# Optimization experiments

Hardware: AMD Instinct MI355X
Metric: run time of the kernel (lower is better)

The kernel has to match this reference:

```python
import jax, jax.numpy as jnp
import numpy as np

B, P, K = 32, 1024, 20  # clouds, points per cloud, kNN neighbors
EPS = 1e-5


def knn_idx(x, k):
    # x: [B,P,d] -> indices of k nearest neighbors (squared L2, includes self), [B,P,k]
    d2 = jnp.sum(x * x, axis=-1)
    dist = d2[:, :, None] + d2[:, None, :] - 2.0 * jnp.einsum('bpd,bqd->bpq', x, x)
    _, idx = jax.lax.top_k(-dist, k)
    return idx


def edge_conv(x, idx, msg_fn):
    # gather neighbor features, build [x_i, x_j - x_i] edge features, max-aggregate
    xj = jax.vmap(lambda xb, ib: xb[ib])(x, idx)            # [B,P,K,d]
    xi = jnp.broadcast_to(x[:, :, None, :], xj.shape)       # [B,P,K,d]
    e = jnp.concatenate([xi, xj - xi], axis=-1)             # [B,P,K,2d]
    return jnp.max(msg_fn(e), axis=2)                       # [B,P,out]


def setup_inputs() -> dict:
    key = jax.random.key(0)
    ks = jax.random.split(key, 5)
    s = 0.05
    return {
        'pos': jax.random.normal(ks[0], (B * P, 3), jnp.float32),
        'W1a': jax.random.normal(ks[1], (6, 64), jnp.float32) * s,
        'b1a': jnp.zeros((64,), jnp.float32),
        'g1': jnp.ones((64,), jnp.float32),
        'be1': jnp.zeros((64,), jnp.float32),
        'W1b': jax.random.normal(ks[2], (64, 64), jnp.float32) * s,
        'b1b': jnp.zeros((64,), jnp.float32),
        'W2': jax.random.normal(ks[3], (128, 128), jnp.float32) * s,
        'b2': jnp.zeros((128,), jnp.float32),
        'Wl': jax.random.normal(ks[4], (192, 128), jnp.float32) * s,
        'bl': jnp.zeros((128,), jnp.float32),
        'batch': jnp.repeat(jnp.arange(B, dtype=jnp.int32), P),
    }


def reference(pos, W1a, b1a, g1, be1, W1b, b1b, W2, b2, Wl, bl, batch):
    # batch is uniform-sized and sorted -> fixed reshape to [B,P,.]
    x0 = pos.reshape(B, P, 3)

    def mlp1(e):  # Linear(6,64) -> BatchNorm -> ReLU -> Linear(64,64)
        h = e @ W1a + b1a
        mu = jnp.mean(h, axis=(0, 1, 2))
        var = jnp.var(h, axis=(0, 1, 2))
        h = (h - mu) * jax.lax.rsqrt(var + EPS) * g1 + be1
        h = jax.nn.relu(h)
        return h @ W1b + b1b

    x1 = edge_conv(x0, knn_idx(x0, K), mlp1)                         # [B,P,64]
    x2 = edge_conv(x1, knn_idx(x1, K), lambda e: e @ W2 + b2)        # [B,P,128]
    h = jnp.concatenate([x1, x2], axis=-1) @ Wl + bl                 # [B,P,128]
    return jnp.max(h, axis=1)                                        # global_max_pool -> [B,128]
```

## Files before the change

kernel.cpp:

```cpp
#include <hip/hip_runtime.h>
#include <cfloat>
#include <cstdint>

#define NB 32
#define NP 1024
#define NK 20
#define NPTS 32768

typedef __attribute__((ext_vector_type(8))) short bf16x8;
typedef __attribute__((ext_vector_type(4))) float f32x4;

__device__ __forceinline__ unsigned bf16rne(float v) {
  const unsigned u = __float_as_uint(v);
  return (u + 0x7fffu + ((u >> 16) & 1u)) >> 16;
}

__global__ __launch_bounds__(256) void kd2(const float* __restrict__ x, int dim,
                                           float* __restrict__ d2) {
  int p = blockIdx.x * 256 + threadIdx.x;
  if (p >= NPTS) return;
  if (dim == 64) {
    const float4* xr = (const float4*)(x + (size_t)p * 64);
    float s = 0.f;
#pragma unroll
    for (int dq = 0; dq < 16; dq++) {
      float4 v = xr[dq];
      s = fmaf(v.x, v.x, s);
      s = fmaf(v.y, v.y, s);
      s = fmaf(v.z, v.z, s);
      s = fmaf(v.w, v.w, s);
    }
    d2[p] = s;
  } else {
    float s = 0.f;
#pragma unroll
    for (int d = 0; d < 3; d++) {
      float v = x[p * 3 + d];
      s = fmaf(v, v, s);
    }
    d2[p] = s;
  }
}

__global__ __launch_bounds__(256) void kxprep(const float* __restrict__ x,
                                              unsigned short* __restrict__ Xh,
                                              unsigned short* __restrict__ Xl) {
  const int t = blockIdx.x * 256 + threadIdx.x;
  const int p = t >> 3, g = t & 7;
  const float4* xr = (const float4*)(x + (size_t)p * 64 + g * 8);
  const float4 v0 = xr[0];
  const float4 v1 = xr[1];
  const float vv[8] = {v0.x, v0.y, v0.z, v0.w, v1.x, v1.y, v1.z, v1.w};
  unsigned short h[8], l[8];
#pragma unroll
  for (int j = 0; j < 8; j++) {
    const float z = vv[j];
    const unsigned u = __float_as_uint(z);
    const unsigned hb = (u + 0x7fffu + ((u >> 16) & 1u)) & 0xffff0000u;
    h[j] = (unsigned short)(hb >> 16);
    l[j] = (unsigned short)bf16rne(z - __uint_as_float(hb));
  }
  const int off = (((p >> 4) * 2 + (g >> 2)) * 64 + ((g & 3) << 4) + (p & 15)) * 8;
  *(uint4*)&Xh[off] = *(const uint4*)&h[0];
  *(uint4*)&Xl[off] = *(const uint4*)&l[0];
}

__global__ __launch_bounds__(256) void kdistm(const unsigned short* __restrict__ Xh,
                                              const unsigned short* __restrict__ Xl,
                                              const float* __restrict__ d2,
                                              int c0, int nc, float* __restrict__ D) {
  const int lane = threadIdx.x & 63;
  const int w = threadIdx.x >> 6;
  const int cloud = blockIdx.x % nc;
  const int t = blockIdx.x / nc;
  const int tr0 = (t >> 3) * 128, tc0 = (t & 7) * 128;
  const int cb = (c0 + cloud) * 1024;
  const int rw = tr0 + w * 32;

  bf16x8 Ah[2][2], Al[2][2];
#pragma unroll
  for (int mt = 0; mt < 2; mt++)
#pragma unroll
    for (int ks = 0; ks < 2; ks++) {
      const int tg = (cb + rw + mt * 16) >> 4;
      const size_t base = ((size_t)(tg * 2 + ks) * 64 + lane) * 8;
      Ah[mt][ks] = *(const bf16x8*)&Xh[base];
      Al[mt][ks] = *(const bf16x8*)&Xl[base];
    }
  float d2r[2][4];
#pragma unroll
  for (int mt = 0; mt < 2; mt++)
#pragma unroll
    for (int r = 0; r < 4; r++)
      d2r[mt][r] = d2[cb + rw + mt * 16 + (lane >> 4) * 4 + r];

  for (int nt = 0; nt < 8; nt++) {
    const int cg = cb + tc0 + nt * 16;
    bf16x8 Bh2[2], Bl2[2];
#pragma unroll
    for (int ks = 0; ks < 2; ks++) {
      const int tg = cg >> 4;
      const size_t base = ((size_t)(tg * 2 + ks) * 64 + lane) * 8;
      Bh2[ks] = *(const bf16x8*)&Xh[base];
      Bl2[ks] = *(const bf16x8*)&Xl[base];
    }
    const float d2c = d2[cg + (lane & 15)];
#pragma unroll
    for (int mt = 0; mt < 2; mt++) {
      f32x4 C = {0.f, 0.f, 0.f, 0.f};
      C = __builtin_amdgcn_mfma_f32_16x16x32_bf16(Ah[mt][0], Bh2[0], C, 0, 0, 0);
      C = __builtin_amdgcn_mfma_f32_16x16x32_bf16(Ah[mt][0], Bl2[0], C, 0, 0, 0);
      C = __builtin_amdgcn_mfma_f32_16x16x32_bf16(Al[mt][0], Bh2[0], C, 0, 0, 0);
      C = __builtin_amdgcn_mfma_f32_16x16x32_bf16(Ah[mt][1], Bh2[1], C, 0, 0, 0);
      C = __builtin_amdgcn_mfma_f32_16x16x32_bf16(Ah[mt][1], Bl2[1], C, 0, 0, 0);
      C = __builtin_amdgcn_mfma_f32_16x16x32_bf16(Al[mt][1], Bh2[1], C, 0, 0, 0);
#pragma unroll
      for (int r = 0; r < 4; r++) {
        const int row = cloud * 1024 + rw + mt * 16 + (lane >> 4) * 4 + r;
        const int col = tc0 + nt * 16 + (lane & 15);
        D[(size_t)row * 1024 + col] = fmaf(-2.f, C[r], d2r[mt][r] + d2c);
      }
    }
  }
}

__device__ __forceinline__ void select20(const float* dv, unsigned long long* w,
                                         int lane, int pg, int gbase,
                                         int* __restrict__ idxo) {
  unsigned k32[16];
#pragma unroll
  for (int ii = 0; ii < 16; ii++) {
    unsigned u = __float_as_uint(dv[ii]);
    u ^= (((int)u >> 31) | 0x80000000u);
    k32[ii] = u;
  }
  unsigned lmn = k32[0];
#pragma unroll
  for (int ii = 1; ii < 16; ii++) lmn = k32[ii] < lmn ? k32[ii] : lmn;
  unsigned mn = lmn, mxm = lmn;
#pragma unroll
  for (int s = 1; s < 64; s <<= 1) {
    const unsigned a = __shfl_xor(mn, s, 64);
    const unsigned b = __shfl_xor(mxm, s, 64);
    mn = a < mn ? a : mn;
    mxm = b > mxm ? b : mxm;
  }
  unsigned lo = mn;
  unsigned long long hi = (unsigned long long)mxm + 1;
  unsigned m32 = 0;
  bool found = false;
  for (int it = 0; it < 34; ++it) {
    if (hi - lo <= 1) break;
    const unsigned m = (unsigned)(lo + ((hi - (unsigned long long)lo) >> 1));
    int cnt = 0;
#pragma unroll
    for (int ii = 0; ii < 16; ii++) cnt += __popcll(__ballot(k32[ii] < m));
    if (cnt < 20)
      lo = m;
    else if (cnt > 63)
      hi = m;
    else {
      m32 = m;
      found = true;
      break;
    }
  }

  if (found) {
    unsigned mask = 0;
    unsigned long long key64[16];
#pragma unroll
    for (int i = 0; i < 4; i++)
#pragma unroll
      for (int j = 0; j < 4; j++) {
        const int ii = i * 4 + j;
        key64[ii] = ((unsigned long long)k32[ii] << 10) |
                    (unsigned)(i * 256 + (lane << 2) + j);
        mask |= (k32[ii] < m32) ? (1u << ii) : 0u;
      }
    const int lc = __popc(mask);
    int x = lc;
#pragma unroll
    for (int s = 1; s < 64; s <<= 1) {
      const int y = __shfl_up(x, s, 64);
      if (lane >= s) x += y;
    }
    int off = x - lc;
    w[lane] = ~0ULL;
    __builtin_amdgcn_wave_barrier();
#pragma unroll
    for (int ii = 0; ii < 16; ii++) {
      if (mask & (1u << ii)) {
        w[off] = key64[ii];
        off++;
      }
    }
    __builtin_amdgcn_wave_barrier();
    const unsigned long long K = w[lane];
    unsigned long long lo64 = ((unsigned long long)lo) << 10;
    unsigned long long hi64 = ((unsigned long long)m32) << 10;
    unsigned long long cut = hi64;
    for (int it = 0; it < 48 && (hi64 - lo64) > 1; ++it) {
      const unsigned long long m = lo64 + ((hi64 - lo64) >> 1);
      const int cnt = __popcll(__ballot(K < m));
      if (cnt == 20) {
        cut = m;
        break;
      }
      if (cnt < 20)
        lo64 = m;
      else
        hi64 = m;
      cut = hi64;
    }
    const unsigned long long sel = __ballot(K < cut);
    if (K < cut) {
      const int slot = __builtin_amdgcn_mbcnt_hi(
          (unsigned)(sel >> 32), __builtin_amdgcn_mbcnt_lo((unsigned)sel, 0));
      idxo[(size_t)pg * NK + slot] = gbase + (int)(K & 1023u);
    }
  } else {
    unsigned long long key64[16];
#pragma unroll
    for (int i = 0; i < 4; i++)
#pragma unroll
      for (int j = 0; j < 4; j++) {
        const int ii = i * 4 + j;
        key64[ii] = ((unsigned long long)k32[ii] << 10) |
                    (unsigned)(i * 256 + (lane << 2) + j);
      }
    unsigned long long lo64 = ((unsigned long long)lo) << 10;
    unsigned long long hi64 = hi << 10;
    unsigned long long cut = hi64;
    for (int it = 0; it < 48 && (hi64 - lo64) > 1; ++it) {
      const unsigned long long m = lo64 + ((hi64 - lo64) >> 1);
      int cnt = 0;
#pragma unroll
      for (int ii = 0; ii < 16; ii++) cnt += __popcll(__ballot(key64[ii] < m));
      if (cnt == 20) {
        cut = m;
        break;
      }
      if (cnt < 20)
        lo64 = m;
      else
        hi64 = m;
      cut = hi64;
    }
    int base = 0;
#pragma unroll
    for (int ii = 0; ii < 16; ii++) {
      const unsigned long long b = __ballot(key64[ii] < cut);
      if (key64[ii] < cut) {
        const int slot = base + __builtin_amdgcn_mbcnt_hi(
                                    (unsigned)(b >> 32),
                                    __builtin_amdgcn_mbcnt_lo((unsigned)b, 0));
        idxo[(size_t)pg * NK + slot] = gbase + (int)(key64[ii] & 1023u);
      }
      base += __popcll(b);
    }
  }
}

__global__ __launch_bounds__(256) void kfsel1(const float* __restrict__ pos,
                                              const float* __restrict__ d2,
                                              int* __restrict__ idxo) {
  __shared__ float px[1024], py[1024], pz[1024], pd2[1024];
  __shared__ unsigned long long lw[4][64];
  const int tid = threadIdx.x;
  const int lane = tid & 63;
  const int w = tid >> 6;
  const int cloud = blockIdx.x >> 6;
  const int mb = blockIdx.x & 63;
  const int cb = cloud << 10;

  {
    const float4* ppos = (const float4*)(pos + (size_t)cb * 3 + tid * 12);
    const float4 a = ppos[0], b = ppos[1], c = ppos[2];
    *(float4*)&px[tid * 4] = make_float4(a.x, a.w, b.z, c.y);
    *(float4*)&py[tid * 4] = make_float4(a.y, b.x, b.w, c.z);
    *(float4*)&pz[tid * 4] = make_float4(a.z, b.y, c.x, c.w);
    *(float4*)&pd2[tid * 4] = *(const float4*)(d2 + cb + tid * 4);
  }
  __syncthreads();

  for (int pp = 0; pp < 4; pp++) {
    const int pl = mb * 16 + w * 4 + pp;
    const float xi0 = px[pl], xi1 = py[pl], xi2 = pz[pl];
    const float dp = pd2[pl];
    float dv[16];
#pragma unroll
    for (int i = 0; i < 4; i++) {
      const float4 X = *(const float4*)&px[i * 256 + lane * 4];
      const float4 Y = *(const float4*)&py[i * 256 + lane * 4];
      const float4 Z = *(const float4*)&pz[i * 256 + lane * 4];
      const float4 Q = *(const float4*)&pd2[i * 256 + lane * 4];
      const float xs[4] = {X.x, X.y, X.z, X.w};
      const float ys[4] = {Y.x, Y.y, Y.z, Y.w};
      const float zs[4] = {Z.x, Z.y, Z.z, Z.w};
      const float qs[4] = {Q.x, Q.y, Q.z, Q.w};
#pragma unroll
      for (int j = 0; j < 4; j++) {
        float acc = 0.f;
        acc = fmaf(xi0, xs[j], acc);
        acc = fmaf(xi1, ys[j], acc);
        acc = fmaf(xi2, zs[j], acc);
        dv[i * 4 + j] = fmaf(-2.f, acc, dp + qs[j]);
      }
    }
    select20(dv, lw[w], lane, cb + pl, cb, idxo);
  }
}

__global__ __launch_bounds__(256) void kselect2(const float* __restrict__ D,
                                                int c0, int* __restrict__ idxo) {
  __shared__ unsigned long long lw[4][64];
  const int lane = threadIdx.x & 63;
  const int sub = threadIdx.x >> 6;
  const int pchunk = blockIdx.x * 4 + sub;
  const int pg = c0 * 1024 + pchunk;
  const int gbase = (pg >> 10) << 10;

  float dv[16];
  const float4* dr = (const float4*)(D + (size_t)pchunk * 1024 + lane * 4);
#pragma unroll
  for (int i = 0; i < 4; i++) {
    const float4 d4 = dr[i * 64];
    dv[i * 4 + 0] = d4.x;
    dv[i * 4 + 1] = d4.y;
    dv[i * 4 + 2] = d4.z;
    dv[i * 4 + 3] = d4.w;
  }
  select20(dv, lw[sub], lane, pg, gbase, idxo);
}

__global__ __launch_bounds__(256) void kstats(const float* __restrict__ pos,
                                              const int* __restrict__ idx,
                                              double* __restrict__ Spart) {
  __shared__ float red[4][42];
  const int tid = threadIdx.x;
  const int w = tid >> 6;
  int p = blockIdx.x * 256 + tid;
  float xi0 = pos[p * 3], xi1 = pos[p * 3 + 1], xi2 = pos[p * 3 + 2];
  float s1[6];
  float s2[36];
#pragma unroll
  for (int a = 0; a < 6; a++) s1[a] = 0.f;
#pragma unroll
  for (int a = 0; a < 36; a++) s2[a] = 0.f;
  for (int k = 0; k < NK; k++) {
    int j = idx[p * NK + k];
    float e[6];
    e[0] = xi0;
    e[1] = xi1;
    e[2] = xi2;
    e[3] = pos[j * 3] - xi0;
    e[4] = pos[j * 3 + 1] - xi1;
    e[5] = pos[j * 3 + 2] - xi2;
#pragma unroll
    for (int a = 0; a < 6; a++) {
      s1[a] += e[a];
#pragma unroll
      for (int b = 0; b < 6; b++) s2[a * 6 + b] = fmaf(e[a], e[b], s2[a * 6 + b]);
    }
  }
#pragma unroll
  for (int a = 0; a < 6; a++) {
#pragma unroll
    for (int m = 1; m < 64; m <<= 1) s1[a] += __shfl_xor(s1[a], m, 64);
  }
#pragma unroll
  for (int a = 0; a < 36; a++) {
#pragma unroll
    for (int m = 1; m < 64; m <<= 1) s2[a] += __shfl_xor(s2[a], m, 64);
  }
  if ((tid & 63) == 0) {
#pragma unroll
    for (int a = 0; a < 6; a++) red[w][a] = s1[a];
#pragma unroll
    for (int a = 0; a < 36; a++) red[w][6 + a] = s2[a];
  }
  __syncthreads();
  if (tid < 42) {
    double t = (double)red[0][tid] + (double)red[1][tid] + (double)red[2][tid] +
               (double)red[3][tid];
    Spart[(size_t)blockIdx.x * 42 + tid] = t;
  }
}

__global__ void kbn(const double* __restrict__ Spart, const float* __restrict__ W1a,
                    const float* __restrict__ b1a, const float* __restrict__ g1,
                    const float* __restrict__ be1, const float* __restrict__ W1b,
                    float* __restrict__ ss, unsigned short* __restrict__ Bh,
                    unsigned short* __restrict__ Bl) {
  __shared__ double S[42];
  const int c = threadIdx.x;
  if (c < 42) {
    double t = 0.0;
    for (int b = 0; b < 128; b++) t += Spart[(size_t)b * 42 + c];
    S[c] = t;
  }
  for (int t = c; t < 4096; t += 256) {
    const int j = t & 7, L = (t >> 3) & 63, f = t >> 9;
    const int nt = f >> 1, ks = f & 1;
    const int k = ks * 32 + (L >> 4) * 8 + j;
    const int n = nt * 16 + (L & 15);
    const float wv = W1b[k * 64 + n];
    const unsigned u = __float_as_uint(wv);
    const unsigned hb = (u + 0x7fffu + ((u >> 16) & 1u)) & 0xffff0000u;
    Bh[t] = (unsigned short)(hb >> 16);
    Bl[t] = (unsigned short)bf16rne(wv - __uint_as_float(hb));
  }
  __syncthreads();
  if (c < 64) {
    double w[6];
#pragma unroll
    for (int d = 0; d < 6; d++) w[d] = (double)W1a[d * 64 + c];
    double b = (double)b1a[c];
    const double invN = 1.0 / (double)((size_t)NPTS * NK);
    double m1 = 0.0;
#pragma unroll
    for (int d = 0; d < 6; d++) m1 += w[d] * S[d];
    m1 *= invN;
    double q = 0.0;
#pragma unroll
    for (int a = 0; a < 6; a++)
#pragma unroll
      for (int d = 0; d < 6; d++) q += w[a] * w[d] * S[6 + a * 6 + d];
    q *= invN;
    double mu = m1 + b;
    double eh2 = q + 2.0 * b * m1 + b * b;
    double var = eh2 - mu * mu;
    if (var < 0.0) var = 0.0;
    double inv = 1.0 / sqrt(var + 1e-5);
    double sc = (double)g1[c] * inv;
    ss[c] = (float)sc;
    ss[64 + c] = (float)((double)be1[c] - mu * sc);
  }
}

#define EC1P 8
__global__ __launch_bounds__(256) void kec1(const float* __restrict__ pos,
                                            const int* __restrict__ idx,
                                            const float* __restrict__ ss,
                                            const float* __restrict__ W1a,
                                            const float* __restrict__ b1a,
                                            const unsigned short* __restrict__ Bh,
                                            const unsigned short* __restrict__ Bl,
                                            const float* __restrict__ b1b,
                                            float* __restrict__ x1) {
  __shared__ __align__(16) unsigned short Ah[4][3072];
  __shared__ __align__(16) unsigned short Al[4][3072];
  __shared__ float nbr[4][160];
  const int tid = threadIdx.x;
  const int lane = tid & 63;
  const int w = tid >> 6;
  const int p0 = blockIdx.x * EC1P + w * 2;

  unsigned short* ah = Ah[w];
  unsigned short* al = Al[w];
  float* nb = nbr[w];

  if (lane < 40) {
    const int j = idx[(size_t)p0 * NK + lane];
    nb[lane * 4 + 0] = pos[j * 3 + 0];
    nb[lane * 4 + 1] = pos[j * 3 + 1];
    nb[lane * 4 + 2] = pos[j * 3 + 2];
  }

  float wdf[3], wbt[3];
#pragma unroll
  for (int d = 0; d < 3; d++) {
    const float top = W1a[d * 64 + lane];
    const float bot = W1a[(3 + d) * 64 + lane];
    wdf[d] = top - bot;
    wbt[d] = bot;
  }
  const float b1 = b1a[lane];
  const float sc = ss[lane];
  const float sh = ss[64 + lane];
  const int lanepart = ((lane >> 5) * 512) + (((lane & 31) >> 3) * 128) + (lane & 7);
  __builtin_amdgcn_wave_barrier();

#pragma unroll
  for (int pp = 0; pp < 2; pp++) {
    const int p = p0 + pp;
    const float xi0 = pos[p * 3], xi1 = pos[p * 3 + 1], xi2 = pos[p * 3 + 2];
    const float pu = fmaf(xi2, wdf[2], fmaf(xi1, wdf[1], fmaf(xi0, wdf[0], b1)));
    for (int k = 0; k < NK; k++) {
      const int row = pp * NK + k;
      const float4 nbv = *(const float4*)&nb[row * 4];
      const float pv = fmaf(nbv.z, wbt[2], fmaf(nbv.y, wbt[1], nbv.x * wbt[0]));
      const float z = fmaxf(fmaf(pu + pv, sc, sh), 0.f);
      const unsigned u = __float_as_uint(z);
      const unsigned hb = (u + 0x7fffu + ((u >> 16) & 1u)) & 0xffff0000u;
      const int off = (row >> 4) * 1024 + (row & 15) * 8 + lanepart;
      ah[off] = (unsigned short)(hb >> 16);
      al[off] = (unsigned short)bf16rne(z - __uint_as_float(hb));
    }
  }
  __builtin_amdgcn_wave_barrier();

  bf16x8 bh[4][2], bl[4][2];
#pragma unroll
  for (int nt = 0; nt < 4; nt++)
#pragma unroll
    for (int ks = 0; ks < 2; ks++) {
      const int base = ((nt * 2 + ks) * 64 + lane) * 8;
      bh[nt][ks] = *(const bf16x8*)&Bh[base];
      bl[nt][ks] = *(const bf16x8*)&Bl[base];
    }

  float pA[4], pB[4];
#pragma unroll
  for (int nt = 0; nt < 4; nt++) {
    pA[nt] = -FLT_MAX;
    pB[nt] = -FLT_MAX;
  }
  const int q4 = (lane >> 4) * 4;

#pragma unroll
  for (int mt = 0; mt < 3; mt++) {
    const bf16x8 a_h0 = *(const bf16x8*)&ah[mt * 1024 + lane * 8];
    const bf16x8 a_l0 = *(const bf16x8*)&al[mt * 1024 + lane * 8];
    const bf16x8 a_h1 = *(const bf16x8*)&ah[mt * 1024 + 512 + lane * 8];
    const bf16x8 a_l1 = *(const bf16x8*)&al[mt * 1024 + 512 + lane * 8];
#pragma unroll
    for (int nt = 0; nt < 4; nt++) {
      f32x4 C = {0.f, 0.f, 0.f, 0.f};
      C = __builtin_amdgcn_mfma_f32_16x16x32_bf16(a_h0, bh[nt][0], C, 0, 0, 0);
      C = __builtin_amdgcn_mfma_f32_16x16x32_bf16(a_h0, bl[nt][0], C, 0, 0, 0);
      C = __builtin_amdgcn_mfma_f32_16x16x32_bf16(a_l0, bh[nt][0], C, 0, 0, 0);
      C = __builtin_amdgcn_mfma_f32_16x16x32_bf16(a_h1, bh[nt][1], C, 0, 0, 0);
      C = __builtin_amdgcn_mfma_f32_16x16x32_bf16(a_h1, bl[nt][1], C, 0, 0, 0);
      C = __builtin_amdgcn_mfma_f32_16x16x32_bf16(a_l1, bh[nt][1], C, 0, 0, 0);
#pragma unroll
      for (int r = 0; r < 4; r++) {
        const int row = mt * 16 + q4 + r;
        const float vv = C[r];
        if (row < NK) pA[nt] = fmaxf(pA[nt], vv);
        if (row >= NK && row < 2 * NK) pB[nt] = fmaxf(pB[nt], vv);
      }
    }
  }
#pragma unroll
  for (int s = 16; s < 64; s <<= 1) {
#pragma unroll
    for (int nt = 0; nt < 4; nt++) {
      pA[nt] = fmaxf(pA[nt], __shfl_xor(pA[nt], s, 64));
      pB[nt] = fmaxf(pB[nt], __shfl_xor(pB[nt], s, 64));
    }
  }
  if (lane < 16) {
#pragma unroll
    for (int nt = 0; nt < 4; nt++) {
      const float bb = b1b[nt * 16 + lane];
      x1[(size_t)p0 * 64 + nt * 16 + lane] = pA[nt] + bb;
      x1[(size_t)(p0 + 1) * 64 + nt * 16 + lane] = pB[nt] + bb;
    }
  }
}

__global__ __launch_bounds__(256) void kv(const float* __restrict__ x1,
                                          const float* __restrict__ W2,
                                          float* __restrict__ v) {
  const int c = threadIdx.x & 127;
  const int sub = threadIdx.x >> 7;
  float wv[64];
#pragma unroll
  for (int d = 0; d < 64; d++) wv[d] = W2[(64 + d) * 128 + c];
  const int pbase = blockIdx.x * 64 + sub * 32;
  for (int i = 0; i < 32; i++) {
    const int p = pbase + i;
    const float4* xr = (const float4*)(x1 + (size_t)p * 64);
    float a0 = 0.f, a1 = 0.f;
#pragma unroll
    for (int dq = 0; dq < 16; dq++) {
      float4 xv = xr[dq];
      a0 = fmaf(xv.x, wv[dq * 4 + 0], a0);
      a1 = fmaf(xv.y, wv[dq * 4 + 1], a1);
      a0 = fmaf(xv.z, wv[dq * 4 + 2], a0);
      a1 = fmaf(xv.w, wv[dq * 4 + 3], a1);
    }
    v[(size_t)p * 128 + c] = a0 + a1;
  }
}

__global__ __launch_bounds__(256) void kprep(const float* __restrict__ W2,
                                             const float* __restrict__ Wl,
                                             const float* __restrict__ b2,
                                             const float* __restrict__ bl,
                                             float* __restrict__ Bc,
                                             float* __restrict__ cb) {
  const int t = blockIdx.x * 256 + threadIdx.x;
  const int d = t >> 7, c = t & 127;
  float s = Wl[d * 128 + c];
  for (int e = 0; e < 128; e++)
    s = fmaf(W2[d * 128 + e] - W2[(64 + d) * 128 + e], Wl[(64 + e) * 128 + c], s);
  Bc[d * 128 + c] = s;
  Bc[(64 + 2 * d) * 128 + c] = Wl[(64 + 2 * d) * 128 + c];
  Bc[(64 + 2 * d + 1) * 128 + c] = Wl[(64 + 2 * d + 1) * 128 + c];
  if (d == 0) {
    float sb = bl[c];
    for (int e = 0; e < 128; e++) sb = fmaf(b2[e], Wl[(64 + e) * 128 + c], sb);
    cb[c] = sb;
  }
}

#define ATS 72
#define BSS 132
__global__ __launch_bounds__(256) void kgemm(const float* __restrict__ x1,
                                             const float* __restrict__ v,
                                             const int* __restrict__ idx,
                                             const float* __restrict__ Bc,
                                             float* __restrict__ partial) {
  __shared__ float AT[192 * ATS];
  __shared__ float BS[16 * BSS];
  int* idxs = (int*)BS;
  const int tid = threadIdx.x;
  const int cloud = blockIdx.x & 31;
  const int mb = blockIdx.x >> 5;
  const int pbase = cloud * 1024 + mb * 64;

#pragma unroll
  for (int r = 0; r < 5; r++) {
    int id = r * 256 + tid;
    idxs[id] = idx[(size_t)pbase * NK + id];
  }
#pragma unroll
  for (int r = 0; r < 16; r++) {
    int id = r * 256 + tid;
    int m = id >> 6, k = id & 63;
    AT[k * ATS + m] = x1[(size_t)(pbase + m) * 64 + k];
  }
  __syncthreads();
#pragma unroll
  for (int r = 0; r < 32; r++) {
    int id = r * 256 + tid;
    int m = id >> 7, kk = id & 127;
    const int* ip = &idxs[m * NK];
    float mx = -FLT_MAX;
#pragma unroll
    for (int k = 0; k < NK; k++) mx = fmaxf(mx, v[(size_t)ip[k] * 128 + kk]);
    AT[(64 + kk) * ATS + m] = mx;
  }
  __syncthreads();

  const int tr = tid >> 4, tc = tid & 15;
  float acc[4][8];
#pragma unroll
  for (int i = 0; i < 4; i++)
#pragma unroll
    for (int n = 0; n < 8; n++) acc[i][n] = 0.f;
  for (int kc = 0; kc < 12; kc++) {
#pragma unroll
    for (int r = 0; r < 8; r++) {
      int id = r * 256 + tid;
      int row = id >> 7, col = id & 127;
      BS[row * BSS + col] = Bc[(size_t)(kc * 16 + row) * 128 + col];
    }
    __syncthreads();
#pragma unroll
    for (int k = 0; k < 16; k++) {
      int kg = kc * 16 + k;
      float4 a = *(const float4*)&AT[kg * ATS + tr * 4];
      float4 b0 = *(const float4*)&BS[k * BSS + tc * 8];
      float4 b1 = *(const float4*)&BS[k * BSS + tc * 8 + 4];
      float av[4] = {a.x, a.y, a.z, a.w};
      float bv[8] = {b0.x, b0.y, b0.z, b0.w, b1.x, b1.y, b1.z, b1.w};
#pragma unroll
      for (int i = 0; i < 4; i++)
#pragma unroll
        for (int n = 0; n < 8; n++) acc[i][n] = fmaf(av[i], bv[n], acc[i][n]);
    }
    __syncthreads();
  }
#pragma unroll
  for (int n = 0; n < 8; n++) {
    float m4 = fmaxf(fmaxf(acc[0][n], acc[1][n]), fmaxf(acc[2][n], acc[3][n]));
    BS[tr * BSS + tc * 8 + n] = m4;
  }
  __syncthreads();
  if (tid < 128) {
    float m = -FLT_MAX;
#pragma unroll
    for (int rr = 0; rr < 16; rr++) m = fmaxf(m, BS[rr * BSS + tid]);
    partial[(size_t)(cloud * 16 + mb) * 128 + tid] = m;
  }
}

__global__ __launch_bounds__(256) void kred(const float* __restrict__ partial,
                                            const float* __restrict__ cb,
                                            float* __restrict__ out) {
  int t = blockIdx.x * 256 + threadIdx.x;
  int b = t >> 7, c = t & 127;
  float m = -FLT_MAX;
#pragma unroll
  for (int mb = 0; mb < 16; mb++) m = fmaxf(m, partial[(size_t)(b * 16 + mb) * 128 + c]);
  out[t] = m + cb[c];
}

extern "C" void kernel_launch(void* const* d_in, const int* in_sizes, int n_in,
                              void* d_out, int out_size, void* d_ws, size_t ws_size,
                              hipStream_t stream) {
  const float* pos = (const float*)d_in[0];
  const float* W1a = (const float*)d_in[1];
  const float* b1a = (const float*)d_in[2];
  const float* g1 = (const float*)d_in[3];
  const float* be1 = (const float*)d_in[4];
  const float* W1b = (const float*)d_in[5];
  const float* b1b = (const float*)d_in[6];
  const float* W2 = (const float*)d_in[7];
  const float* b2 = (const float*)d_in[8];
  const float* Wl = (const float*)d_in[9];
  const float* bl = (const float*)d_in[10];
  float* out = (float*)d_out;

  float* ws = (float*)d_ws;
  float* x1 = ws;
  float* v = ws + 2097152;
  int* idx = (int*)(ws + 6291456);
  float* d2b = ws + 6946816;
  double* Spart = (double*)(ws + 6979584);
  float* Bc = ws + 6990336;
  float* cb = ws + 7014912;
  float* ss = ws + 7015040;
  unsigned short* Bh = (unsigned short*)(ws + 7015168);
  unsigned short* Bl = (unsigned short*)(ws + 7017216);
  float* partial = ws + 7019264;
  unsigned short* Xfh = (unsigned short*)(ws + 7084800);
  unsigned short* Xfl = (unsigned short*)(ws + 8133376);
  const size_t base = 9181952;
  float* D = ws + base;

  if (ws_size < (base + 1024 * 1024) * sizeof(float)) return;

  size_t avail = ws_size / sizeof(float) - base;
  int nc = 1;
  for (int c = 32; c >= 1; c >>= 1)
    if ((size_t)c * 1024 * 1024 <= avail) {
      nc = c;
      break;
    }

  kd2<<<128, 256, 0, stream>>>(pos, 3, d2b);
  kfsel1<<<NB * 64, 256, 0, stream>>>(pos, d2b, idx);

  kstats<<<128, 256, 0, stream>>>(pos, idx, Spart);
  kbn<<<1, 256, 0, stream>>>(Spart, W1a, b1a, g1, be1, W1b, ss, Bh, Bl);
  kec1<<<NPTS / EC1P, 256, 0, stream>>>(pos, idx, ss, W1a, b1a, Bh, Bl, b1b, x1);

  kd2<<<128, 256, 0, stream>>>(x1, 64, d2b);
  kxprep<<<1024, 256, 0, stream>>>(x1, Xfh, Xfl);
  for (int c0 = 0; c0 < NB; c0 += nc) {
    kdistm<<<nc * 64, 256, 0, stream>>>(Xfh, Xfl, d2b, c0, nc, D);
    kselect2<<<nc * 256, 256, 0, stream>>>(D, c0, idx);
  }

  kv<<<512, 256, 0, stream>>>(x1, W2, v);
  kprep<<<32, 256, 0, stream>>>(W2, Wl, b2, bl, Bc, cb);
  kgemm<<<512, 256, 0, stream>>>(x1, v, idx, Bc, partial);
  kred<<<16, 256, 0, stream>>>(partial, cb, out);
}
```

Measured before the change: 352.8 us.

## Use interpolation-guided threshold search and bitonic sort in kNN top-20 selection

The first six steps of the top-20 threshold search now pick the pivot by interpolating in float space toward a target count, instead of plain bisection, so the candidate window of at most 64 is reached in fewer ballot passes. Once candidates are compacted into shared memory, a 64-lane bitonic sort replaces the second 64-bit bisection loop, and the first 20 lanes write their indices in sorted order. kfsel1 also moves to 512-thread blocks with one query point per wave, dropping the per-wave loop over four points. Costs: the bitonic sort is a fixed 21 shuffle stages, the interpolation constants (42 and 140) are heuristics for the candidate-count distribution, and the 64-bit keys are now rebuilt on the fly in the fallback path.

Measured after the change: 340.7 us. 1.04x faster.

```diff
diff --git a/kernel.cpp b/kernel.cpp
--- a/kernel.cpp
+++ b/kernel.cpp
@@ -13,6 +13,11 @@
 __device__ __forceinline__ unsigned bf16rne(float v) {
   const unsigned u = __float_as_uint(v);
   return (u + 0x7fffu + ((u >> 16) & 1u)) >> 16;
+}
+
+__device__ __forceinline__ float unsort_f(unsigned s) {
+  const unsigned m = (~(unsigned)((int)s >> 31)) | 0x80000000u;
+  return __uint_as_float(s ^ m);
 }
 
 __global__ __launch_bounds__(256) void kd2(const float* __restrict__ x, int dim,
@@ -137,29 +142,47 @@
   unsigned lmn = k32[0];
 #pragma unroll
   for (int ii = 1; ii < 16; ii++) lmn = k32[ii] < lmn ? k32[ii] : lmn;
-  unsigned mn = lmn, mxm = lmn;
+  unsigned mn = lmn, mlm = lmn;
 #pragma unroll
   for (int s = 1; s < 64; s <<= 1) {
     const unsigned a = __shfl_xor(mn, s, 64);
-    const unsigned b = __shfl_xor(mxm, s, 64);
+    const unsigned b = __shfl_xor(mlm, s, 64);
     mn = a < mn ? a : mn;
-    mxm = b > mxm ? b : mxm;
-  }
-  unsigned lo = mn;
-  unsigned long long hi = (unsigned long long)mxm + 1;
+    mlm = b > mlm ? b : mlm;
+  }
+  unsigned lo32 = mn;
+  unsigned long long hi32 = (unsigned long long)mlm + 1;
+  float flo = unsort_f(mn), fhi = unsort_f(mlm);
+  float clo = 0.f, chi = 140.f;
   unsigned m32 = 0;
   bool found = false;
-  for (int it = 0; it < 34; ++it) {
-    if (hi - lo <= 1) break;
-    const unsigned m = (unsigned)(lo + ((hi - (unsigned long long)lo) >> 1));
+  for (int it = 0; it < 40; ++it) {
+    if (hi32 - (unsigned long long)lo32 <= 1) break;
+    unsigned m;
+    if (it < 6) {
+      float fr = (42.f - clo) / (chi - clo);
+      fr = fr < 0.04f ? 0.04f : (fr > 0.96f ? 0.96f : fr);
+      const float pf = fmaf(fhi - flo, fr, flo);
+      unsigned u = __float_as_uint(pf);
+      u ^= (((int)u >> 31) | 0x80000000u);
+      m = u;
+      if (m <= lo32) m = lo32 + 1;
+      if ((unsigned long long)m >= hi32) m = (unsigned)(hi32 - 1);
+    } else {
+      m = (unsigned)(lo32 + ((hi32 - lo32) >> 1));
+    }
     int cnt = 0;
 #pragma unroll
     for (int ii = 0; ii < 16; ii++) cnt += __popcll(__ballot(k32[ii] < m));
-    if (cnt < 20)
-      lo = m;
-    else if (cnt > 63)
-      hi = m;
-    else {
+    if (cnt < 20) {
+      lo32 = m;
+      flo = unsort_f(m);
+      clo = (float)cnt;
+    } else if (cnt > 64) {
+      hi32 = m;
+      fhi = unsort_f(m);
+      chi = (float)cnt;
+    } else {
       m32 = m;
       found = true;
       break;
@@ -168,16 +191,8 @@
 
   if (found) {
     unsigned mask = 0;
-    unsigned long long key64[16];
-#pragma unroll
-    for (int i = 0; i < 4; i++)
-#pragma unroll
-      for (int j = 0; j < 4; j++) {
-        const int ii = i * 4 + j;
-        key64[ii] = ((unsigned long long)k32[ii] << 10) |
-                    (unsigned)(i * 256 + (lane << 2) + j);
-        mask |= (k32[ii] < m32) ? (1u << ii) : 0u;
-      }
+#pragma unroll
+    for (int ii = 0; ii < 16; ii++) mask |= (k32[ii] < m32) ? (1u << ii) : 0u;
     const int lc = __popc(mask);
     int x = lc;
 #pragma unroll
@@ -189,20 +204,45 @@
     w[lane] = ~0ULL;
     __builtin_amdgcn_wave_barrier();
 #pragma unroll
-    for (int ii = 0; ii < 16; ii++) {
-      if (mask & (1u << ii)) {
-        w[off] = key64[ii];
-        off++;
+    for (int i = 0; i < 4; i++)
+#pragma unroll
+      for (int j = 0; j < 4; j++) {
+        const int ii = i * 4 + j;
+        if ((mask & (1u << ii)) && off < 64) {
+          w[off] = ((unsigned long long)k32[ii] << 10) |
+                   (unsigned)(i * 256 + (lane << 2) + j);
+          off++;
+        }
       }
-    }
     __builtin_amdgcn_wave_barrier();
-    const unsigned long long K = w[lane];
-    unsigned long long lo64 = ((unsigned long long)lo) << 10;
-    unsigned long long hi64 = ((unsigned long long)m32) << 10;
+    unsigned long long K = w[lane];
+#pragma unroll
+    for (int k = 2; k <= 64; k <<= 1) {
+#pragma unroll
+      for (int j2 = k >> 1; j2 > 0; j2 >>= 1) {
+        const unsigned long long o = __shfl_xor(K, j2, 64);
+        const bool takeMin = (((lane & j2) == 0) == ((lane & k) == 0));
+        const bool lt = K < o;
+        const unsigned long long sml = lt ? K : o;
+        const unsigned long long big = lt ? o : K;
+        K = takeMin ? sml : big;
+      }
+    }
+    if (lane < NK) idxo[(size_t)pg * NK + lane] = gbase + (int)(K & 1023u);
+  } else {
+    unsigned long long lo64 = ((unsigned long long)lo32) << 10;
+    unsigned long long hi64 = hi32 << 10;
     unsigned long long cut = hi64;
     for (int it = 0; it < 48 && (hi64 - lo64) > 1; ++it) {
       const unsigned long long m = lo64 + ((hi64 - lo64) >> 1);
-      const int cnt = __popcll(__ballot(K < m));
+      int cnt = 0;
+#pragma unroll
+      for (int ii = 0; ii < 16; ii++) {
+        const unsigned long long key =
+            ((unsigned long long)k32[ii] << 10) |
+            (unsigned)(((ii >> 2) << 8) + (lane << 2) + (ii & 3));
+        cnt += __popcll(__ballot(key < m));
+      }
       if (cnt == 20) {
         cut = m;
         break;
@@ -213,103 +253,70 @@
         hi64 = m;
       cut = hi64;
     }
-    const unsigned long long sel = __ballot(K < cut);
-    if (K < cut) {
-      const int slot = __builtin_amdgcn_mbcnt_hi(
-          (unsigned)(sel >> 32), __builtin_amdgcn_mbcnt_lo((unsigned)sel, 0));
-      idxo[(size_t)pg * NK + slot] = gbase + (int)(K & 1023u);
-    }
-  } else {
-    unsigned long long key64[16];
-#pragma unroll
-    for (int i = 0; i < 4; i++)
-#pragma unroll
-      for (int j = 0; j < 4; j++) {
-        const int ii = i * 4 + j;
-        key64[ii] = ((unsigned long long)k32[ii] << 10) |
-                    (unsigned)(i * 256 + (lane << 2) + j);
-      }
-    unsigned long long lo64 = ((unsigned long long)lo) << 10;
-    unsigned long long hi64 = hi << 10;
-    unsigned long long cut = hi64;
-    for (int it = 0; it < 48 && (hi64 - lo64) > 1; ++it) {
-      const unsigned long long m = lo64 + ((hi64 - lo64) >> 1);
-      int cnt = 0;
-#pragma unroll
-      for (int ii = 0; ii < 16; ii++) cnt += __popcll(__ballot(key64[ii] < m));
-      if (cnt == 20) {
-        cut = m;
-        break;
-      }
-      if (cnt < 20)
-        lo64 = m;
-      else
-        hi64 = m;
-      cut = hi64;
-    }
     int base = 0;
 #pragma unroll
     for (int ii = 0; ii < 16; ii++) {
-      const unsigned long long b = __ballot(key64[ii] < cut);
-      if (key64[ii] < cut) {
+      const unsigned long long key =
+          ((unsigned long long)k32[ii] << 10) |
+          (unsigned)(((ii >> 2) << 8) + (lane << 2) + (ii & 3));
+      const unsigned long long b = __ballot(key < cut);
+      if (key < cut) {
         const int slot = base + __builtin_amdgcn_mbcnt_hi(
                                     (unsigned)(b >> 32),
                                     __builtin_amdgcn_mbcnt_lo((unsigned)b, 0));
-        idxo[(size_t)pg * NK + slot] = gbase + (int)(key64[ii] & 1023u);
+        idxo[(size_t)pg * NK + slot] = gbase + (int)(key & 1023u);
       }
       base += __popcll(b);
     }
   }
 }
 
-__global__ __launch_bounds__(256) void kfsel1(const float* __restrict__ pos,
+__global__ __launch_bounds__(512) void kfsel1(const float* __restrict__ pos,
                                               const float* __restrict__ d2,
                                               int* __restrict__ idxo) {
   __shared__ float px[1024], py[1024], pz[1024], pd2[1024];
-  __shared__ unsigned long long lw[4][64];
+  __shared__ unsigned long long lw[8][64];
   const int tid = threadIdx.x;
   const int lane = tid & 63;
   const int w = tid >> 6;
-  const int cloud = blockIdx.x >> 6;
-  const int mb = blockIdx.x & 63;
+  const int cloud = blockIdx.x >> 7;
+  const int mb = blockIdx.x & 127;
   const int cb = cloud << 10;
 
-  {
+  if (tid < 256) {
     const float4* ppos = (const float4*)(pos + (size_t)cb * 3 + tid * 12);
     const float4 a = ppos[0], b = ppos[1], c = ppos[2];
     *(float4*)&px[tid * 4] = make_float4(a.x, a.w, b.z, c.y);
     *(float4*)&py[tid * 4] = make_float4(a.y, b.x, b.w, c.z);
     *(float4*)&pz[tid * 4] = make_float4(a.z, b.y, c.x, c.w);
-    *(float4*)&pd2[tid * 4] = *(const float4*)(d2 + cb + tid * 4);
-  }
+  }
+  *(float2*)&pd2[tid * 2] = *(const float2*)(d2 + cb + tid * 2);
   __syncthreads();
 
-  for (int pp = 0; pp < 4; pp++) {
-    const int pl = mb * 16 + w * 4 + pp;
-    const float xi0 = px[pl], xi1 = py[pl], xi2 = pz[pl];
-    const float dp = pd2[pl];
-    float dv[16];
-#pragma unroll
-    for (int i = 0; i < 4; i++) {
-      const float4 X = *(const float4*)&px[i * 256 + lane * 4];
-      const float4 Y = *(const float4*)&py[i * 256 + lane * 4];
-      const float4 Z = *(const float4*)&pz[i * 256 + lane * 4];
-      const float4 Q = *(const float4*)&pd2[i * 256 + lane * 4];
-      const float xs[4] = {X.x, X.y, X.z, X.w};
-      const float ys[4] = {Y.x, Y.y, Y.z, Y.w};
-      const float zs[4] = {Z.x, Z.y, Z.z, Z.w};
-      const float qs[4] = {Q.x, Q.y, Q.z, Q.w};
-#pragma unroll
-      for (int j = 0; j < 4; j++) {
-        float acc = 0.f;
-        acc = fmaf(xi0, xs[j], acc);
-        acc = fmaf(xi1, ys[j], acc);
-        acc = fmaf(xi2, zs[j], acc);
-        dv[i * 4 + j] = fmaf(-2.f, acc, dp + qs[j]);
-      }
-    }
-    select20(dv, lw[w], lane, cb + pl, cb, idxo);
-  }
+  const int pl = mb * 8 + w;
+  const float xi0 = px[pl], xi1 = py[pl], xi2 = pz[pl];
+  const float dp = pd2[pl];
+  float dv[16];
+#pragma unroll
+  for (int i = 0; i < 4; i++) {
+    const float4 X = *(const float4*)&px[i * 256 + lane * 4];
+    const float4 Y = *(const float4*)&py[i * 256 + lane * 4];
+    const float4 Z = *(const float4*)&pz[i * 256 + lane * 4];
+    const float4 Q = *(const float4*)&pd2[i * 256 + lane * 4];
+    const float xs[4] = {X.x, X.y, X.z, X.w};
+    const float ys[4] = {Y.x, Y.y, Y.z, Y.w};
+    const float zs[4] = {Z.x, Z.y, Z.z, Z.w};
+    const float qs[4] = {Q.x, Q.y, Q.z, Q.w};
+#pragma unroll
+    for (int j = 0; j < 4; j++) {
+      float acc = 0.f;
+      acc = fmaf(xi0, xs[j], acc);
+      acc = fmaf(xi1, ys[j], acc);
+      acc = fmaf(xi2, zs[j], acc);
+      dv[i * 4 + j] = fmaf(-2.f, acc, dp + qs[j]);
+    }
+  }
+  select20(dv, lw[w], lane, cb + pl, cb, idxo);
 }
 
 __global__ __launch_bounds__(256) void kselect2(const float* __restrict__ D,
@@ -744,7 +751,7 @@
     }
 
   kd2<<<128, 256, 0, stream>>>(pos, 3, d2b);
-  kfsel1<<<NB * 64, 256, 0, stream>>>(pos, d2b, idx);
+  kfsel1<<<NB * 128, 512, 0, stream>>>(pos, d2b, idx);
 
   kstats<<<128, 256, 0, stream>>>(pos, idx, Spart);
   kbn<<<1, 256, 0, stream>>>(Spart, W1a, b1a, g1, be1, W1b, ss, Bh, Bl);
```
